# Kernel tuning notes

Hardware: AMD Instinct MI355X
Metric: run time of the kernel (lower is better)

## Reference

```python
import jax, jax.numpy as jnp
import numpy as np

NEG_SLOPE = 0.01


def _pos(x):
    return jnp.where(x > 0, x, jnp.zeros_like(x))


def _neg(x):
    return jnp.where(x < 0, x, jnp.zeros_like(x))


def setup_inputs() -> dict:
    N = 4096
    key = jax.random.key(0)
    k1, k2, k3, k4, k5, k6 = jax.random.split(key, 6)
    x = jax.random.normal(k1, (1, N), dtype=jnp.float32)
    eps = 0.1
    lb0 = x - eps
    ub0 = x + eps
    scale = 1.0 / np.sqrt(N)
    W1 = jax.random.normal(k2, (N, N), dtype=jnp.float32) * scale
    b1 = jax.random.normal(k3, (1, N), dtype=jnp.float32)
    W2 = jax.random.normal(k4, (N, N), dtype=jnp.float32) * scale
    b2 = jax.random.normal(k5, (1, N), dtype=jnp.float32)
    raw_alpha = jax.random.normal(k6, (N,), dtype=jnp.float32)
    return {"lb0": lb0, "ub0": ub0, "W1": W1, "b1": b1, "W2": W2, "b2": b2, "raw_alpha": raw_alpha}


def reference(lb0, ub0, W1, b1, W2, b2, raw_alpha):
    N = raw_alpha.shape[0]
    ns = NEG_SLOPE
    # ---- backsubstitution: fold layer2 transformer through layer1 (affine: lslope=uslope=W1) ----
    clslope, clintercept, cuslope, cuintercept = W2, b2, W2, b2
    clp, cln = _pos(clslope), _neg(clslope)
    cup, cun = _pos(cuslope), _neg(cuslope)
    clintercept = b1 @ clp.T + b1 @ cln.T + clintercept  # [1,N]
    cuintercept = b1 @ cup.T + b1 @ cun.T + cuintercept
    clslope = clp @ W1 + cln @ W1  # [N,N]
    cuslope = cup @ W1 + cun @ W1
    # ---- certifier against initial interval bounds ----
    lsp, lsn = _pos(clslope), _neg(clslope)
    usp, usn = _pos(cuslope), _neg(cuslope)
    lbounds = lb0 @ lsp.T + ub0 @ lsn.T + clintercept  # [1,N]
    ubounds = ub0 @ usp.T + lb0 @ usn.T + cuintercept
    # ---- DeepPoly LeakyReLU relaxation (neg_slope <= 1 branch) ----
    alpha = jax.nn.sigmoid(raw_alpha)
    slope = ((ubounds - lbounds * ns) / (ubounds - lbounds)).reshape(-1)  # [N]
    slope = jnp.where(jnp.isnan(slope), jnp.zeros_like(slope), slope)
    intercept = (1.0 - slope) * ubounds  # [1,N]
    ones = jnp.ones((N,), dtype=lbounds.dtype)
    zeros_row = jnp.zeros((1, N), dtype=lbounds.dtype)
    lslope, lintercept = ones, zeros_row
    uslope, uintercept = ones, zeros_row
    below = (ubounds <= 0).reshape(-1)
    above = (lbounds >= 0).reshape(-1)
    lslope = jnp.where(below, ns * ones, lslope)
    uslope = jnp.where(below, ns * ones, uslope)
    lslope = jnp.where(above, ones, lslope)
    uslope = jnp.where(above, ones, uslope)
    crossing = ~(below | above)
    uslope = jnp.where(crossing, slope, uslope)
    uintercept = jnp.where(crossing, intercept, uintercept)
    lslope_v1 = jnp.where(crossing, ones, lslope)
    lslope_v2 = jnp.where(crossing, ns * ones, lslope)
    lslope = alpha * lslope_v1 + (1.0 - alpha) * lslope_v2
    return jnp.diag(lslope), lintercept, jnp.diag(uslope), uintercept
```

## Files before the change

kernel.cpp:

```cpp
#include <hip/hip_runtime.h>
#include <stdint.h>

#define NN 4096
#define NEG_SLOPE 0.01f

typedef _Float16 f16x8 __attribute__((ext_vector_type(8)));
typedef _Float16 f16x4 __attribute__((ext_vector_type(4)));
typedef float f32x4 __attribute__((ext_vector_type(4)));

__device__ __forceinline__ void async_ld16(void* lds, const void* g) {
    __builtin_amdgcn_global_load_lds(
        (__attribute__((address_space(1))) const void*)(const void*)g,
        (__attribute__((address_space(3))) void*)lds, 16, 0, 0);
}

__global__ __launch_bounds__(256, 4)
void gemm_S(const _Float16* __restrict__ Ah, const _Float16* __restrict__ Bt,
            const float* __restrict__ lb0, const float* __restrict__ ub0,
            float* __restrict__ S) {
    __shared__ _Float16 sA[128][64];
    __shared__ _Float16 sB[128][64];
    const int t = threadIdx.x;
    const int lane = t & 63;
    const int w = t >> 6;
    const int waveRow = w >> 1, waveCol = w & 1;
    const int quad = lane >> 4, l15 = lane & 15, l7 = lane & 7;

    const int bRow = (blockIdx.x >> 5) * 128;
    const int bCol = (blockIdx.x & 31) * 128;

    const int rOff = lane >> 3;
    const int uG   = (lane & 7) ^ (lane >> 3);
    const _Float16* gA = Ah + (size_t)(bRow + w * 32 + rOff) * NN + uG * 8;
    const _Float16* gB = Bt + (size_t)(bCol + w * 32 + rOff) * NN + uG * 8;

    f32x4 acc[4][4];
#pragma unroll
    for (int i = 0; i < 4; ++i)
#pragma unroll
        for (int j = 0; j < 4; ++j) acc[i][j] = (f32x4){0.f, 0.f, 0.f, 0.f};

    for (int kt = 0; kt < NN / 64; ++kt) {
        const int k0 = kt * 64;
        __syncthreads();
#pragma unroll
        for (int i = 0; i < 4; ++i) {
            async_ld16(&sA[w * 32 + i * 8][0], gA + (size_t)(i * 8) * NN + k0);
            async_ld16(&sB[w * 32 + i * 8][0], gB + (size_t)(i * 8) * NN + k0);
        }
        __syncthreads();

#pragma unroll
        for (int s = 0; s < 2; ++s) {
            f16x8 af[4];
#pragma unroll
            for (int fr = 0; fr < 4; ++fr) {
                const int r = waveRow * 64 + fr * 16 + l15;
                af[fr] = *(const f16x8*)&sA[r][((s * 4 + quad) ^ l7) * 8];
            }
#pragma unroll
            for (int fc = 0; fc < 4; ++fc) {
                const int c = waveCol * 64 + fc * 16 + l15;
                const f16x8 bf = *(const f16x8*)&sB[c][((s * 4 + quad) ^ l7) * 8];
#pragma unroll
                for (int fr = 0; fr < 4; ++fr)
                    acc[fr][fc] = __builtin_amdgcn_mfma_f32_16x16x32_f16(af[fr], bf, acc[fr][fc], 0, 0, 0);
            }
        }
    }

    float ev[4];
#pragma unroll
    for (int fc = 0; fc < 4; ++fc) {
        const int col = bCol + waveCol * 64 + fc * 16 + l15;
        ev[fc] = 0.5f * (ub0[col] - lb0[col]);
    }
#pragma unroll
    for (int fr = 0; fr < 4; ++fr) {
#pragma unroll
        for (int r = 0; r < 4; ++r) {
            float sv = 0.f;
#pragma unroll
            for (int fc = 0; fc < 4; ++fc)
                sv += ev[fc] * fabsf(acc[fr][fc][r]);
#pragma unroll
            for (int mk = 1; mk < 16; mk <<= 1)
                sv += __shfl_xor(sv, mk, 64);
            if (l15 == 0) {
                const int row = bRow + waveRow * 64 + fr * 16 + quad * 4 + r;
                atomicAdd(&S[row], sv);
            }
        }
    }
}

__global__ __launch_bounds__(256)
void prepB(const float* __restrict__ W1, const float* __restrict__ lb0,
           const float* __restrict__ ub0, _Float16* __restrict__ Bt,
           float* __restrict__ v) {
    __shared__ float sT[64][65];
    const int bi = (blockIdx.x & 63) * 64;
    const int bn = (blockIdx.x >> 6) * 64;
    const int t = threadIdx.x;
    const int r = t >> 4, c4 = (t & 15) * 4;

    const float4 lv = *(const float4*)&lb0[bn + c4];
    const float4 uv = *(const float4*)&ub0[bn + c4];
    const float cw0 = 0.5f * (lv.x + uv.x), cw1 = 0.5f * (lv.y + uv.y);
    const float cw2 = 0.5f * (lv.z + uv.z), cw3 = 0.5f * (lv.w + uv.w);

#pragma unroll
    for (int p = 0; p < 4; ++p) {
        const float4 a = *(const float4*)&W1[(size_t)(bi + r + p * 16) * NN + bn + c4];
        sT[r + p * 16][c4 + 0] = a.x;
        sT[r + p * 16][c4 + 1] = a.y;
        sT[r + p * 16][c4 + 2] = a.z;
        sT[r + p * 16][c4 + 3] = a.w;
        float part = a.x * cw0 + a.y * cw1 + a.z * cw2 + a.w * cw3;
#pragma unroll
        for (int mk = 1; mk < 16; mk <<= 1)
            part += __shfl_xor(part, mk, 64);
        if ((t & 15) == 0) atomicAdd(&v[bi + r + p * 16], part);
    }
    __syncthreads();
    const int n = t >> 4, k4 = (t & 15) * 4;
#pragma unroll
    for (int p = 0; p < 4; ++p) {
        const int nn_ = n + p * 16;
        f16x4 h;
        h[0] = (_Float16)sT[k4 + 0][nn_];
        h[1] = (_Float16)sT[k4 + 1][nn_];
        h[2] = (_Float16)sT[k4 + 2][nn_];
        h[3] = (_Float16)sT[k4 + 3][nn_];
        *(f16x4*)&Bt[(size_t)(bn + nn_) * NN + bi + k4] = h;
    }
}

__global__ __launch_bounds__(256)
void prepA(const float* __restrict__ W2, const float* __restrict__ b1,
           const float* __restrict__ b2, const float* __restrict__ v,
           _Float16* __restrict__ Ah, float* __restrict__ u,
           float* __restrict__ cj, float* __restrict__ S) {
    const int j = blockIdx.x;
    const int t = threadIdx.x;
    const float* row = W2 + (size_t)j * NN;
    _Float16* orow = Ah + (size_t)j * NN;
    float d1 = 0.f, d2 = 0.f;
#pragma unroll
    for (int p = 0; p < 4; ++p) {
        const int i = t * 4 + p * 1024;
        const float4 a = *(const float4*)&row[i];
        const float4 bb = *(const float4*)&b1[i];
        const float4 vv = *(const float4*)&v[i];
        d1 += a.x * bb.x + a.y * bb.y + a.z * bb.z + a.w * bb.w;
        d2 += a.x * vv.x + a.y * vv.y + a.z * vv.z + a.w * vv.w;
        f16x4 h;
        h[0] = (_Float16)a.x; h[1] = (_Float16)a.y;
        h[2] = (_Float16)a.z; h[3] = (_Float16)a.w;
        *(f16x4*)&orow[i] = h;
    }
#pragma unroll
    for (int mk = 1; mk < 64; mk <<= 1) {
        d1 += __shfl_xor(d1, mk, 64);
        d2 += __shfl_xor(d2, mk, 64);
    }
    __shared__ float w1s[4], w2s[4];
    if ((t & 63) == 0) { w1s[t >> 6] = d1; w2s[t >> 6] = d2; }
    __syncthreads();
    if (t == 0) {
        cj[j] = w1s[0] + w1s[1] + w1s[2] + w1s[3] + b2[j];
        u[j]  = w2s[0] + w2s[1] + w2s[2] + w2s[3];
        S[j]  = 0.f;
    }
}

__global__ __launch_bounds__(256)
void write_out(const float* __restrict__ S, const float* __restrict__ u,
               const float* __restrict__ cj, const float* __restrict__ ra,
               float* __restrict__ out) {
    const size_t N2 = (size_t)NN * NN;
    const int b = blockIdx.x;
    const int t = threadIdx.x;
    if (b < 8192) {
        const int j = b & 4095;
        const bool isU = b >= 4096;
        const float base = u[j] + cj[j];
        const float Sv = S[j];
        const float lb = base - Sv, ub = base + Sv;
        const float alpha = 1.f / (1.f + expf(-ra[j]));
        float s = (ub - lb * NEG_SLOPE) / (ub - lb);
        if (!(s == s)) s = 0.f;
        const bool below = (ub <= 0.f), above = (lb >= 0.f);
        const bool crossing = !(below || above);
        const float uslope = crossing ? s : (below ? NEG_SLOPE : 1.f);
        const float v1 = below ? NEG_SLOPE : 1.f;
        const float v2 = crossing ? NEG_SLOPE : v1;
        const float lslope = alpha * v1 + (1.f - alpha) * v2;
        const float dval = isU ? uslope : lslope;
        float4* rowp = (float4*)(out + (isU ? (N2 + NN) : (size_t)0) + (size_t)j * NN);
        const int dq = j >> 2, dr = j & 3;
#pragma unroll
        for (int q = 0; q < 4; ++q) {
            const int i4 = t + q * 256;
            float4 z = make_float4(0.f, 0.f, 0.f, 0.f);
            if (i4 == dq) ((float*)&z)[dr] = dval;
            rowp[i4] = z;
        }
    } else if (b == 8192) {
        float4* rowp = (float4*)(out + N2);
#pragma unroll
        for (int q = 0; q < 4; ++q)
            rowp[t + q * 256] = make_float4(0.f, 0.f, 0.f, 0.f);
    } else {
        float* rowp = out + 2 * N2 + NN;
#pragma unroll
        for (int q = 0; q < 16; ++q) {
            const int j = t + q * 256;
            const float base = u[j] + cj[j];
            const float Sv = S[j];
            const float lb = base - Sv, ub = base + Sv;
            float s = (ub - lb * NEG_SLOPE) / (ub - lb);
            if (!(s == s)) s = 0.f;
            const bool below = (ub <= 0.f), above = (lb >= 0.f);
            const bool crossing = !(below || above);
            rowp[j] = crossing ? (1.f - s) * ub : 0.f;
        }
    }
}

extern "C" void kernel_launch(void* const* d_in, const int* in_sizes, int n_in,
                              void* d_out, int out_size, void* d_ws, size_t ws_size,
                              hipStream_t stream) {
    const float* lb0 = (const float*)d_in[0];
    const float* ub0 = (const float*)d_in[1];
    const float* W1  = (const float*)d_in[2];
    const float* b1  = (const float*)d_in[3];
    const float* W2  = (const float*)d_in[4];
    const float* b2  = (const float*)d_in[5];
    const float* ra  = (const float*)d_in[6];
    float* out = (float*)d_out;

    _Float16* Ahalf = (_Float16*)d_out;
    _Float16* Bt    = Ahalf + (size_t)NN * NN;

    float* v  = (float*)d_ws;
    float* S  = v + NN;
    float* u  = S + NN;
    float* cj = u + NN;

    hipMemsetAsync(v, 0, NN * sizeof(float), stream);
    prepB<<<dim3(4096), dim3(256), 0, stream>>>(W1, lb0, ub0, Bt, v);
    prepA<<<dim3(NN), dim3(256), 0, stream>>>(W2, b1, b2, v, Ahalf, u, cj, S);
    gemm_S<<<dim3(1024), dim3(256), 0, stream>>>(Ahalf, Bt, lb0, ub0, S);
    write_out<<<dim3(8194), dim3(256), 0, stream>>>(S, u, cj, ra, out);
}
```

Baseline: 398.3 us.

## Fuse prep kernels, compute center term in GEMM epilogue, overlap zero-fill with GEMM

Merges the two prep kernels into one launch and drops the memset and the W1·center matvec. The center contribution is instead accumulated in the GEMM epilogue alongside the radius term. The GEMM now also writes the zero-filled upper-diagonal region of the output with nontemporal stores while its main loop runs, so the finish kernel only writes the lower diagonal rows plus sparse diagonal entries. This cuts launches and a separate serial dependency chain, but adds extra atomics and stores inside the GEMM and relies on intricate output offset bookkeeping.

```diff
diff --git a/kernel.cpp b/kernel.cpp
--- a/kernel.cpp
+++ b/kernel.cpp
@@ -7,6 +7,12 @@
 typedef _Float16 f16x8 __attribute__((ext_vector_type(8)));
 typedef _Float16 f16x4 __attribute__((ext_vector_type(4)));
 typedef float f32x4 __attribute__((ext_vector_type(4)));
+
+#define L_DIAG 0
+#define L_INT  16777216
+#define U_DIAG 16781312
+#define U_INT  33558528
+#define TAIL0  33554432
 
 __device__ __forceinline__ void async_ld16(void* lds, const void* g) {
     __builtin_amdgcn_global_load_lds(
@@ -15,9 +21,10 @@
 }
 
 __global__ __launch_bounds__(256, 4)
-void gemm_S(const _Float16* __restrict__ Ah, const _Float16* __restrict__ Bt,
-            const float* __restrict__ lb0, const float* __restrict__ ub0,
-            float* __restrict__ S) {
+void gemm_SU(const _Float16* __restrict__ Ah, const _Float16* __restrict__ Bt,
+             const float* __restrict__ lb0, const float* __restrict__ ub0,
+             float* __restrict__ S, float* __restrict__ U,
+             f32x4* __restrict__ zbase) {
     __shared__ _Float16 sA[128][64];
     __shared__ _Float16 sB[128][64];
     const int t = threadIdx.x;
@@ -40,6 +47,8 @@
 #pragma unroll
         for (int j = 0; j < 4; ++j) acc[i][j] = (f32x4){0.f, 0.f, 0.f, 0.f};
 
+    const f32x4 zv = (f32x4){0.f, 0.f, 0.f, 0.f};
+
     for (int kt = 0; kt < NN / 64; ++kt) {
         const int k0 = kt * 64;
         __syncthreads();
@@ -67,163 +76,179 @@
                     acc[fr][fc] = __builtin_amdgcn_mfma_f32_16x16x32_f16(af[fr], bf, acc[fr][fc], 0, 0, 0);
             }
         }
-    }
-
-    float ev[4];
+
+        if ((kt & 3) == 0) {
+            const int zi = kt >> 2;
+            __builtin_nontemporal_store(zv,
+                zbase + (size_t)blockIdx.x * 4096 + zi * 256 + t);
+        }
+    }
+
+    float ev[4], cv[4];
 #pragma unroll
     for (int fc = 0; fc < 4; ++fc) {
         const int col = bCol + waveCol * 64 + fc * 16 + l15;
-        ev[fc] = 0.5f * (ub0[col] - lb0[col]);
+        const float l = lb0[col], u_ = ub0[col];
+        ev[fc] = 0.5f * (u_ - l);
+        cv[fc] = 0.5f * (u_ + l);
     }
 #pragma unroll
     for (int fr = 0; fr < 4; ++fr) {
 #pragma unroll
         for (int r = 0; r < 4; ++r) {
-            float sv = 0.f;
-#pragma unroll
-            for (int fc = 0; fc < 4; ++fc)
-                sv += ev[fc] * fabsf(acc[fr][fc][r]);
-#pragma unroll
-            for (int mk = 1; mk < 16; mk <<= 1)
+            float sv = 0.f, uv = 0.f;
+#pragma unroll
+            for (int fc = 0; fc < 4; ++fc) {
+                const float m = acc[fr][fc][r];
+                sv += ev[fc] * fabsf(m);
+                uv += cv[fc] * m;
+            }
+#pragma unroll
+            for (int mk = 1; mk < 16; mk <<= 1) {
                 sv += __shfl_xor(sv, mk, 64);
+                uv += __shfl_xor(uv, mk, 64);
+            }
             if (l15 == 0) {
                 const int row = bRow + waveRow * 64 + fr * 16 + quad * 4 + r;
                 atomicAdd(&S[row], sv);
+                atomicAdd(&U[row], uv);
             }
         }
     }
 }
 
 __global__ __launch_bounds__(256)
-void prepB(const float* __restrict__ W1, const float* __restrict__ lb0,
-           const float* __restrict__ ub0, _Float16* __restrict__ Bt,
-           float* __restrict__ v) {
+void prep(const float* __restrict__ W2, const float* __restrict__ W1,
+          const float* __restrict__ b1, const float* __restrict__ b2,
+          _Float16* __restrict__ Ah, _Float16* __restrict__ Bt,
+          float* __restrict__ cj, float* __restrict__ S, float* __restrict__ U) {
     __shared__ float sT[64][65];
-    const int bi = (blockIdx.x & 63) * 64;
-    const int bn = (blockIdx.x >> 6) * 64;
-    const int t = threadIdx.x;
-    const int r = t >> 4, c4 = (t & 15) * 4;
-
-    const float4 lv = *(const float4*)&lb0[bn + c4];
-    const float4 uv = *(const float4*)&ub0[bn + c4];
-    const float cw0 = 0.5f * (lv.x + uv.x), cw1 = 0.5f * (lv.y + uv.y);
-    const float cw2 = 0.5f * (lv.z + uv.z), cw3 = 0.5f * (lv.w + uv.w);
-
-#pragma unroll
-    for (int p = 0; p < 4; ++p) {
-        const float4 a = *(const float4*)&W1[(size_t)(bi + r + p * 16) * NN + bn + c4];
-        sT[r + p * 16][c4 + 0] = a.x;
-        sT[r + p * 16][c4 + 1] = a.y;
-        sT[r + p * 16][c4 + 2] = a.z;
-        sT[r + p * 16][c4 + 3] = a.w;
-        float part = a.x * cw0 + a.y * cw1 + a.z * cw2 + a.w * cw3;
-#pragma unroll
-        for (int mk = 1; mk < 16; mk <<= 1)
-            part += __shfl_xor(part, mk, 64);
-        if ((t & 15) == 0) atomicAdd(&v[bi + r + p * 16], part);
-    }
-    __syncthreads();
-    const int n = t >> 4, k4 = (t & 15) * 4;
-#pragma unroll
-    for (int p = 0; p < 4; ++p) {
-        const int nn_ = n + p * 16;
-        f16x4 h;
-        h[0] = (_Float16)sT[k4 + 0][nn_];
-        h[1] = (_Float16)sT[k4 + 1][nn_];
-        h[2] = (_Float16)sT[k4 + 2][nn_];
-        h[3] = (_Float16)sT[k4 + 3][nn_];
-        *(f16x4*)&Bt[(size_t)(bn + nn_) * NN + bi + k4] = h;
-    }
-}
-
-__global__ __launch_bounds__(256)
-void prepA(const float* __restrict__ W2, const float* __restrict__ b1,
-           const float* __restrict__ b2, const float* __restrict__ v,
-           _Float16* __restrict__ Ah, float* __restrict__ u,
-           float* __restrict__ cj, float* __restrict__ S) {
-    const int j = blockIdx.x;
-    const int t = threadIdx.x;
-    const float* row = W2 + (size_t)j * NN;
-    _Float16* orow = Ah + (size_t)j * NN;
-    float d1 = 0.f, d2 = 0.f;
-#pragma unroll
-    for (int p = 0; p < 4; ++p) {
-        const int i = t * 4 + p * 1024;
-        const float4 a = *(const float4*)&row[i];
-        const float4 bb = *(const float4*)&b1[i];
-        const float4 vv = *(const float4*)&v[i];
-        d1 += a.x * bb.x + a.y * bb.y + a.z * bb.z + a.w * bb.w;
-        d2 += a.x * vv.x + a.y * vv.y + a.z * vv.z + a.w * vv.w;
-        f16x4 h;
-        h[0] = (_Float16)a.x; h[1] = (_Float16)a.y;
-        h[2] = (_Float16)a.z; h[3] = (_Float16)a.w;
-        *(f16x4*)&orow[i] = h;
-    }
-#pragma unroll
-    for (int mk = 1; mk < 64; mk <<= 1) {
-        d1 += __shfl_xor(d1, mk, 64);
-        d2 += __shfl_xor(d2, mk, 64);
-    }
-    __shared__ float w1s[4], w2s[4];
-    if ((t & 63) == 0) { w1s[t >> 6] = d1; w2s[t >> 6] = d2; }
-    __syncthreads();
-    if (t == 0) {
-        cj[j] = w1s[0] + w1s[1] + w1s[2] + w1s[3] + b2[j];
-        u[j]  = w2s[0] + w2s[1] + w2s[2] + w2s[3];
-        S[j]  = 0.f;
-    }
-}
-
-__global__ __launch_bounds__(256)
-void write_out(const float* __restrict__ S, const float* __restrict__ u,
-               const float* __restrict__ cj, const float* __restrict__ ra,
-               float* __restrict__ out) {
-    const size_t N2 = (size_t)NN * NN;
+    __shared__ float w4[4];
     const int b = blockIdx.x;
     const int t = threadIdx.x;
-    if (b < 8192) {
-        const int j = b & 4095;
-        const bool isU = b >= 4096;
-        const float base = u[j] + cj[j];
-        const float Sv = S[j];
-        const float lb = base - Sv, ub = base + Sv;
+    if (b < 4096) {
+        const int j = b;
+        const float* row = W2 + (size_t)j * NN;
+        _Float16* orow = Ah + (size_t)j * NN;
+        float d1 = 0.f;
+#pragma unroll
+        for (int p = 0; p < 4; ++p) {
+            const int i = p * 1024 + t * 4;
+            const float4 a = *(const float4*)&row[i];
+            const float4 bb = *(const float4*)&b1[i];
+            d1 += a.x * bb.x + a.y * bb.y + a.z * bb.z + a.w * bb.w;
+            f16x4 h;
+            h[0] = (_Float16)a.x; h[1] = (_Float16)a.y;
+            h[2] = (_Float16)a.z; h[3] = (_Float16)a.w;
+            *(f16x4*)&orow[i] = h;
+        }
+#pragma unroll
+        for (int mk = 1; mk < 64; mk <<= 1) d1 += __shfl_xor(d1, mk, 64);
+        if ((t & 63) == 0) w4[t >> 6] = d1;
+        __syncthreads();
+        if (t == 0) {
+            cj[j] = w4[0] + w4[1] + w4[2] + w4[3] + b2[j];
+            S[j] = 0.f;
+            U[j] = 0.f;
+        }
+    } else {
+        const int tile = b - 4096;
+        const int bi = (tile & 63) * 64;
+        const int bn = (tile >> 6) * 64;
+        const int r = t >> 4, c4 = (t & 15) * 4;
+#pragma unroll
+        for (int p = 0; p < 4; ++p) {
+            const float4 a = *(const float4*)&W1[(size_t)(bi + r + p * 16) * NN + bn + c4];
+            sT[r + p * 16][c4 + 0] = a.x;
+            sT[r + p * 16][c4 + 1] = a.y;
+            sT[r + p * 16][c4 + 2] = a.z;
+            sT[r + p * 16][c4 + 3] = a.w;
+        }
+        __syncthreads();
+        const int n = t >> 4, k4 = (t & 15) * 4;
+#pragma unroll
+        for (int p = 0; p < 4; ++p) {
+            const int nn_ = n + p * 16;
+            f16x4 h;
+            h[0] = (_Float16)sT[k4 + 0][nn_];
+            h[1] = (_Float16)sT[k4 + 1][nn_];
+            h[2] = (_Float16)sT[k4 + 2][nn_];
+            h[3] = (_Float16)sT[k4 + 3][nn_];
+            *(f16x4*)&Bt[(size_t)(bn + nn_) * NN + bi + k4] = h;
+        }
+    }
+}
+
+__device__ __forceinline__ void get_lub(int j, const float* S, const float* U,
+                                        const float* cj, float& lb, float& ub) {
+    const float base = U[j] + cj[j], Sv = S[j];
+    lb = base - Sv;
+    ub = base + Sv;
+}
+__device__ __forceinline__ float slope_of(float lb, float ub) {
+    float s = (ub - lb * NEG_SLOPE) / (ub - lb);
+    if (!(s == s)) s = 0.f;
+    return s;
+}
+__device__ __forceinline__ float uslope_of(float lb, float ub) {
+    const bool below = (ub <= 0.f), above = (lb >= 0.f);
+    return (!(below || above)) ? slope_of(lb, ub) : (below ? NEG_SLOPE : 1.f);
+}
+
+__global__ __launch_bounds__(256)
+void finish(const float* __restrict__ S, const float* __restrict__ U,
+            const float* __restrict__ cj, const float* __restrict__ ra,
+            float* __restrict__ out) {
+    const int b = blockIdx.x;
+    const int t = threadIdx.x;
+    if (b < 4096) {
+        const int j = b;
+        float lb, ub;
+        get_lub(j, S, U, cj, lb, ub);
         const float alpha = 1.f / (1.f + expf(-ra[j]));
-        float s = (ub - lb * NEG_SLOPE) / (ub - lb);
-        if (!(s == s)) s = 0.f;
         const bool below = (ub <= 0.f), above = (lb >= 0.f);
         const bool crossing = !(below || above);
-        const float uslope = crossing ? s : (below ? NEG_SLOPE : 1.f);
         const float v1 = below ? NEG_SLOPE : 1.f;
         const float v2 = crossing ? NEG_SLOPE : v1;
         const float lslope = alpha * v1 + (1.f - alpha) * v2;
-        const float dval = isU ? uslope : lslope;
-        float4* rowp = (float4*)(out + (isU ? (N2 + NN) : (size_t)0) + (size_t)j * NN);
+        f32x4* rowp = (f32x4*)(out + (size_t)j * NN);
         const int dq = j >> 2, dr = j & 3;
 #pragma unroll
         for (int q = 0; q < 4; ++q) {
             const int i4 = t + q * 256;
-            float4 z = make_float4(0.f, 0.f, 0.f, 0.f);
-            if (i4 == dq) ((float*)&z)[dr] = dval;
-            rowp[i4] = z;
-        }
-    } else if (b == 8192) {
-        float4* rowp = (float4*)(out + N2);
-#pragma unroll
-        for (int q = 0; q < 4; ++q)
-            rowp[t + q * 256] = make_float4(0.f, 0.f, 0.f, 0.f);
+            f32x4 z = (f32x4){0.f, 0.f, 0.f, 0.f};
+            if (i4 == dq) z[dr] = lslope;
+            __builtin_nontemporal_store(z, &rowp[i4]);
+        }
+    } else if (b < 4112) {
+        const int j = (b - 4096) * 256 + t;
+        if (j < 4095) {
+            float lb, ub;
+            get_lub(j, S, U, cj, lb, ub);
+            out[U_DIAG + (size_t)j * NN + j] = uslope_of(lb, ub);
+        }
+    } else if (b == 4112) {
+        f32x4* p = (f32x4*)(out + TAIL0);
+#pragma unroll
+        for (int q = 0; q < 4; ++q) {
+            const int i4 = t + q * 256;
+            f32x4 z = (f32x4){0.f, 0.f, 0.f, 0.f};
+            if (i4 == 1023) {
+                float lb, ub;
+                get_lub(4095, S, U, cj, lb, ub);
+                z[3] = uslope_of(lb, ub);
+            }
+            __builtin_nontemporal_store(z, &p[i4]);
+        }
     } else {
-        float* rowp = out + 2 * N2 + NN;
 #pragma unroll
         for (int q = 0; q < 16; ++q) {
             const int j = t + q * 256;
-            const float base = u[j] + cj[j];
-            const float Sv = S[j];
-            const float lb = base - Sv, ub = base + Sv;
-            float s = (ub - lb * NEG_SLOPE) / (ub - lb);
-            if (!(s == s)) s = 0.f;
+            float lb, ub;
+            get_lub(j, S, U, cj, lb, ub);
             const bool below = (ub <= 0.f), above = (lb >= 0.f);
             const bool crossing = !(below || above);
-            rowp[j] = crossing ? (1.f - s) * ub : 0.f;
+            out[U_INT + j] = crossing ? (1.f - slope_of(lb, ub)) * ub : 0.f;
         }
     }
 }
@@ -240,17 +265,15 @@
     const float* ra  = (const float*)d_in[6];
     float* out = (float*)d_out;
 
-    _Float16* Ahalf = (_Float16*)d_out;
-    _Float16* Bt    = Ahalf + (size_t)NN * NN;
-
-    float* v  = (float*)d_ws;
-    float* S  = v + NN;
-    float* u  = S + NN;
-    float* cj = u + NN;
-
-    hipMemsetAsync(v, 0, NN * sizeof(float), stream);
-    prepB<<<dim3(4096), dim3(256), 0, stream>>>(W1, lb0, ub0, Bt, v);
-    prepA<<<dim3(NN), dim3(256), 0, stream>>>(W2, b1, b2, v, Ahalf, u, cj, S);
-    gemm_S<<<dim3(1024), dim3(256), 0, stream>>>(Ahalf, Bt, lb0, ub0, S);
-    write_out<<<dim3(8194), dim3(256), 0, stream>>>(S, u, cj, ra, out);
-}
+    _Float16* Ah = (_Float16*)d_out;
+    _Float16* Bt = Ah + (size_t)NN * NN;
+
+    float* S  = (float*)d_ws;
+    float* U  = S + NN;
+    float* cj = U + NN;
+
+    prep<<<dim3(8192), dim3(256), 0, stream>>>(W2, W1, b1, b2, Ah, Bt, cj, S, U);
+    gemm_SU<<<dim3(1024), dim3(256), 0, stream>>>(Ah, Bt, lb0, ub0, S, U,
+                                                  (f32x4*)(out + L_INT));
+    finish<<<dim3(4114), dim3(256), 0, stream>>>(S, U, cj, ra, out);
+}
```

Measured after the change: 379.2 us. 4.8% less time.
